# Optimization experiments

Measured on AMD Instinct MI355X. Metric: run time of the kernel, lower is better.

Reference implementation:

```python
import jax, jax.numpy as jnp
import numpy as np

IC, IND, MID, OC, OD, ITERS = 8, 16, 32, 8, 16, 3
B, H, W = 8, 64, 64


def squash(x, axis):
    sq = jnp.sum(x * x, axis=axis, keepdims=True)
    return sq / (0.5 + sq) * x / (jnp.sqrt(sq + 1e-6) + 1e-6)


def gconv(x, w, b, pad):
    # grouped conv over the IC capsule groups (equivalent to the per-capsule
    # Conv2d blocks applied to slices of the capsule axis)
    y = jax.lax.conv_general_dilated(
        x, w, (1, 1), pad,
        dimension_numbers=("NCHW", "OIHW", "NCHW"),
        feature_group_count=IC)
    return y + b[None, :, None, None]


def setup_inputs() -> dict:
    key = jax.random.key(0)
    ks = jax.random.split(key, 7)
    x = jax.random.normal(ks[0], (B, IC * IND, H, W), jnp.float32)
    w1 = jax.random.normal(ks[1], (IC * MID, IND, 1, 1), jnp.float32) * 0.1
    b1 = jax.random.normal(ks[2], (IC * MID,), jnp.float32) * 0.1
    w2 = jax.random.normal(ks[3], (IC * MID, MID, 3, 3), jnp.float32) * 0.05
    b2 = jax.random.normal(ks[4], (IC * MID,), jnp.float32) * 0.1
    w3 = jax.random.normal(ks[5], (IC * OC * OD, MID, 1, 1), jnp.float32) * 0.05
    b3 = jax.random.normal(ks[6], (IC * OC * OD,), jnp.float32) * 0.1
    attn_w = jnp.zeros((1, OC, 1, 1, 1), jnp.float32)  # torch init: zeros
    attn_b = jnp.ones((1, OC, 1, 1, 1), jnp.float32)   # torch init: ones
    return dict(x=x, w1=w1, b1=b1, w2=w2, b2=b2, w3=w3, b3=b3,
                attn_w=attn_w, attn_b=attn_b)


def reference(x, w1, b1, w2, b2, w3, b3, attn_w, attn_b):
    bsz = x.shape[0]
    h_, w_ = x.shape[-2], x.shape[-1]
    # per-capsule conv stack: ReLU -> 1x1 -> ReLU -> 3x3 -> ReLU -> 1x1
    h = jax.nn.relu(x)
    h = jax.nn.relu(gconv(h, w1, b1, "VALID"))
    h = jax.nn.relu(gconv(h, w2, b2, "SAME"))
    h = gconv(h, w3, b3, "VALID")                     # [B, IC*OC*OD, H, W]
    u_hat = h.reshape(bsz, IC, OC, OD, h_, w_)
    u_sq = squash(u_hat, axis=3)
    # dynamic routing
    b = jnp.zeros((bsz, IC, OC, h_, w_), u_hat.dtype)
    for _ in range(ITERS - 1):
        c = jax.nn.sigmoid(b)
        s = jnp.sum(u_sq * c[:, :, :, None], axis=1)   # [B, OC, OD, H, W]
        v = squash(s, axis=2)
        b = b + jnp.sum(u_sq * v[:, None], axis=3)     # [B, IC, OC, H, W]
    c = jax.nn.sigmoid(b)
    s = jnp.sum(u_hat * c[:, :, :, None], axis=1)      # [B, OC, OD, H, W]
    # SpatialCapsuleAttn
    mean_hw = jnp.mean(s, axis=(-2, -1), keepdims=True)        # adaptive avg pool(1)
    avg = jnp.sum(s * mean_hw, axis=2)                         # [B, OC, H, W]
    t = avg.reshape(bsz, OC, h_ * w_)
    m = jnp.mean(t, axis=-1, keepdims=True)
    sd = jnp.std(t, axis=-1, keepdims=True, ddof=1) + 1e-6     # torch std: unbiased
    t = (t - m) / sd
    t = t.reshape(bsz, OC, 1, h_, w_) * attn_w + attn_b
    s = s * jax.nn.sigmoid(t)
    out = s.reshape(bsz, OC * OD, h_, w_) + x
    return out
```

## Files before the change

### kernel.cpp

```cpp
#include <hip/hip_runtime.h>
#include <hip/hip_bf16.h>
#include <hip/hip_fp16.h>

#define HW 4096

typedef _Float16 f16x8 __attribute__((ext_vector_type(8)));
typedef float f32x4 __attribute__((ext_vector_type(4)));

#define FOR8(X) X(0) X(1) X(2) X(3) X(4) X(5) X(6) X(7)

static __device__ __forceinline__ __half2 u2h(unsigned int u) {
    union { unsigned int u; __half2 h; } c; c.u = u; return c.h;
}
static __device__ __forceinline__ unsigned int h2u(__half2 h) {
    union { unsigned int u; __half2 h; } c; c.h = h; return c.u;
}
static __device__ __forceinline__ f16x8 uint4_as_f16x8(uint4 v) {
    union { uint4 u; f16x8 f; } c; c.u = v; return c.f;
}

__global__ __launch_bounds__(256) void k0b_w3h(const float* __restrict__ w3, ushort* __restrict__ w3h) {
    int gi = blockIdx.x * 256 + threadIdx.x;
    if (gi >= 32768) return;
    int j = gi & 7;
    int l = (gi >> 3) & 63;
    int p = gi >> 9;
    int ic = p >> 3, oc = p & 7;
    int od = l & 15;
    int m  = ((l >> 4) << 3) + j;
    __half h = __float2half(w3[(size_t)((ic * 128 + oc * 16 + od) * 32 + m)]);
    w3h[gi] = __half_as_ushort(h);
}

__global__ __launch_bounds__(256) void k0c_w2f(const float* __restrict__ w2, ushort* __restrict__ w2f) {
    int gi = blockIdx.x * 256 + threadIdx.x;
    if (gi >= 73728) return;
    int j   = gi & 7;
    int l   = (gi >> 3) & 63;
    int h   = (gi >> 9) & 1;
    int tap = (gi >> 10) % 9;
    int g   = gi / 9216;
    int co = h * 16 + (l & 15);
    int ci = ((l >> 4) << 3) + j;
    float v = w2[(size_t)((g * 32 + co) * 32 + ci) * 9 + tap];
    w2f[gi] = __half_as_ushort(__float2half(v));
}

__global__ __launch_bounds__(256) void k1_conv1(const float* __restrict__ x, const float* __restrict__ w1,
                                                const float* __restrict__ b1, ushort* __restrict__ h1g) {
    int bi = blockIdx.x;
    int chunk = bi & 15;
    int g = (bi >> 4) & 7;
    int b = bi >> 7;
    int pos = chunk * 256 + threadIdx.x;

    const float* xb = x + (size_t)(b * 128 + g * 16) * HW + pos;
    float xv[16];
#pragma unroll
    for (int i = 0; i < 16; ++i) xv[i] = fmaxf(xb[i * HW], 0.f);

    const float* wg = w1 + g * 32 * 16;
    const float* bg = b1 + g * 32;
    ushort hv[32];
#pragma unroll
    for (int m = 0; m < 32; ++m) {
        float acc = bg[m];
#pragma unroll
        for (int i = 0; i < 16; ++i) acc = fmaf(xv[i], wg[m * 16 + i], acc);
        hv[m] = __half_as_ushort(__float2half(fmaxf(acc, 0.f)));
    }
    ushort* hb = h1g + ((size_t)(b * 8 + g) * HW + pos) * 32;
#pragma unroll
    for (int q = 0; q < 4; ++q) *(uint4*)&hb[q * 8] = *(uint4*)&hv[q * 8];
}

__global__ __launch_bounds__(256) void k2_conv2(const ushort* __restrict__ h1g, const ushort* __restrict__ w2f,
                                                const float* __restrict__ b2, ushort* __restrict__ h2g) {
    int bi = blockIdx.x;
    int pt = bi & 63;
    int g  = (bi >> 6) & 7;
    int b  = bi >> 9;
    int t  = threadIdx.x;
    int w  = t >> 6, l = t & 63;
    int pxbase = pt * 64 + w * 16;
    int kgrp = l >> 4;

    int y = pxbase >> 6;
    int x = (pxbase & 63) + (l & 15);

    const ushort* hbase = h1g + (size_t)(b * 8 + g) * HW * 32;
    f16x8 Bf[9];
#pragma unroll
    for (int dy = -1; dy <= 1; ++dy) {
        int yy = y + dy;
        int yyc = yy < 0 ? 0 : (yy > 63 ? 63 : yy);
        bool rv = (yy >= 0) && (yy < 64);
#pragma unroll
        for (int dx = -1; dx <= 1; ++dx) {
            int xx = x + dx;
            int xc = xx < 0 ? 0 : (xx > 63 ? 63 : xx);
            uint4 v = *(const uint4*)&hbase[((yyc << 6) + xc) * 32 + kgrp * 8];
            bool ok = rv && (xx >= 0) && (xx < 64);
            v.x = ok ? v.x : 0u; v.y = ok ? v.y : 0u;
            v.z = ok ? v.z : 0u; v.w = ok ? v.w : 0u;
            Bf[(dy + 1) * 3 + (dx + 1)] = uint4_as_f16x8(v);
        }
    }

    const ushort* wg = w2f + (size_t)g * 9216;
    f16x8 Af[9][2];
#pragma unroll
    for (int tap = 0; tap < 9; ++tap)
#pragma unroll
        for (int h = 0; h < 2; ++h)
            Af[tap][h] = *(const f16x8*)&wg[((tap * 2 + h) * 64 + l) * 8];

    f32x4 acc[2];
#pragma unroll
    for (int h = 0; h < 2; ++h) {
        float4 bias = *(const float4*)(b2 + g * 32 + h * 16 + kgrp * 4);
        acc[h][0] = bias.x; acc[h][1] = bias.y; acc[h][2] = bias.z; acc[h][3] = bias.w;
    }
#pragma unroll
    for (int tap = 0; tap < 9; ++tap) {
#pragma unroll
        for (int h = 0; h < 2; ++h)
            acc[h] = __builtin_amdgcn_mfma_f32_16x16x32_f16(Af[tap][h], Bf[tap], acc[h], 0, 0, 0);
    }

    int px = pxbase + (l & 15);
    ushort* ob = h2g + ((size_t)(b * 8 + g) * HW + px) * 32;
#pragma unroll
    for (int h = 0; h < 2; ++h) {
        __half2 lo = __floats2half2_rn(fmaxf(acc[h][0], 0.f), fmaxf(acc[h][1], 0.f));
        __half2 hi = __floats2half2_rn(fmaxf(acc[h][2], 0.f), fmaxf(acc[h][3], 0.f));
        uint2 wv; wv.x = h2u(lo); wv.y = h2u(hi);
        *(uint2*)&ob[h * 16 + kgrp * 4] = wv;
    }
}

__global__ __launch_bounds__(512) void k3f_route(const ushort* __restrict__ h2g, const ushort* __restrict__ w3h,
                                                 const float* __restrict__ b3, ushort* __restrict__ sOut,
                                                 float* __restrict__ part) {
    __shared__ ushort us[32 * 1024];
    __shared__ float wred[8][16][8];
    int bid = blockIdx.x;
    int b   = bid >> 7;
    int px0 = (bid & 127) << 5;
    int t   = threadIdx.x;
    int w   = t >> 6, l = t & 63;

    {
        int ic = w;
        int lrow = l & 15, lk = l >> 4;
        f16x8 bf0 = *(const f16x8*)&h2g[(((size_t)(b * 8 + ic)) * HW + px0 + lrow) * 32 + lk * 8];
        f16x8 bf1 = *(const f16x8*)&h2g[(((size_t)(b * 8 + ic)) * HW + px0 + 16 + lrow) * 32 + lk * 8];
        int s0sw = (lrow & 15) << 3;
#pragma unroll
        for (int oc = 0; oc < 8; ++oc) {
            f16x8 af = *(const f16x8*)&w3h[((ic * 8 + oc) * 64 + l) * 8];
            float4 bv = *(const float4*)(b3 + ic * 128 + oc * 16 + lk * 4);
            f32x4 c0; c0[0] = bv.x; c0[1] = bv.y; c0[2] = bv.z; c0[3] = bv.w;
            int ch = ic * 128 + oc * 16 + lk * 4;
            f32x4 d0 = __builtin_amdgcn_mfma_f32_16x16x32_f16(af, bf0, c0, 0, 0, 0);
            uint2 wv0;
            wv0.x = h2u(__floats2half2_rn(d0[0], d0[1]));
            wv0.y = h2u(__floats2half2_rn(d0[2], d0[3]));
            *(uint2*)&us[lrow * 1024 + (ch ^ s0sw)] = wv0;
            f32x4 d1 = __builtin_amdgcn_mfma_f32_16x16x32_f16(af, bf1, c0, 0, 0, 0);
            uint2 wv1;
            wv1.x = h2u(__floats2half2_rn(d1[0], d1[1]));
            wv1.y = h2u(__floats2half2_rn(d1[2], d1[3]));
            *(uint2*)&us[(16 + lrow) * 1024 + (ch ^ s0sw)] = wv1;
        }
    }
    __syncthreads();

    int px  = t >> 4;
    int oc  = (t >> 1) & 7;
    int odh = t & 1;
    int ssw = (px & 15) << 3;
    const ushort* ur = &us[px * 1024];
#define LDQ(i) uint4 q##i = *(const uint4*)&ur[((i) * 128 + oc * 16 + odh * 8) ^ ssw];
    FOR8(LDQ)
#undef LDQ
    __syncthreads();

#define UNP(i) float2 f0 = __half22float2(u2h(q##i.x)), f1 = __half22float2(u2h(q##i.y)), \
                      f2 = __half22float2(u2h(q##i.z)), f3 = __half22float2(u2h(q##i.w));

#define SC(i) float sc##i; { UNP(i) \
        float sp = f0.x*f0.x + f0.y*f0.y + f1.x*f1.x + f1.y*f1.y \
                 + f2.x*f2.x + f2.y*f2.y + f3.x*f3.x + f3.y*f3.y; \
        sp += __shfl_xor(sp, 1); \
        sc##i = sp / ((0.5f + sp) * (sqrtf(sp + 1e-6f) + 1e-6f)); }
    FOR8(SC)
#undef SC

#define BRI(i) float br##i = 0.f;
    FOR8(BRI)
#undef BRI

    float s0, s1, s2, s3, s4, s5, s6, s7;
#pragma unroll
    for (int it = 0; it < 2; ++it) {
#define CSC(i) float cs##i = sc##i / (1.f + __expf(-br##i));
        FOR8(CSC)
#undef CSC
        s0 = s1 = s2 = s3 = s4 = s5 = s6 = s7 = 0.f;
#define SVA(i) { UNP(i) \
        s0 = fmaf(f0.x, cs##i, s0); s1 = fmaf(f0.y, cs##i, s1); \
        s2 = fmaf(f1.x, cs##i, s2); s3 = fmaf(f1.y, cs##i, s3); \
        s4 = fmaf(f2.x, cs##i, s4); s5 = fmaf(f2.y, cs##i, s5); \
        s6 = fmaf(f3.x, cs##i, s6); s7 = fmaf(f3.y, cs##i, s7); }
        FOR8(SVA)
#undef SVA
        float sp = s0*s0 + s1*s1 + s2*s2 + s3*s3 + s4*s4 + s5*s5 + s6*s6 + s7*s7;
        sp += __shfl_xor(sp, 1);
        float f = sp / ((0.5f + sp) * (sqrtf(sp + 1e-6f) + 1e-6f));
#define DOTD(i) { UNP(i) \
        float dp = f0.x*s0 + f0.y*s1 + f1.x*s2 + f1.y*s3 + f2.x*s4 + f2.y*s5 + f3.x*s6 + f3.y*s7; \
        dp += __shfl_xor(dp, 1); \
        br##i = fmaf(sc##i * f, dp, br##i); }
        FOR8(DOTD)
#undef DOTD
    }

#define CF(i) float cf##i = 1.f / (1.f + __expf(-br##i));
    FOR8(CF)
#undef CF
    s0 = s1 = s2 = s3 = s4 = s5 = s6 = s7 = 0.f;
#define FS(i) { UNP(i) \
        s0 = fmaf(f0.x, cf##i, s0); s1 = fmaf(f0.y, cf##i, s1); \
        s2 = fmaf(f1.x, cf##i, s2); s3 = fmaf(f1.y, cf##i, s3); \
        s4 = fmaf(f2.x, cf##i, s4); s5 = fmaf(f2.y, cf##i, s5); \
        s6 = fmaf(f3.x, cf##i, s6); s7 = fmaf(f3.y, cf##i, s7); }
    FOR8(FS)
#undef FS
#undef UNP

    {
        uint4 pk;
        pk.x = h2u(__floats2half2_rn(s0, s1));
        pk.y = h2u(__floats2half2_rn(s2, s3));
        pk.z = h2u(__floats2half2_rn(s4, s5));
        pk.w = h2u(__floats2half2_rn(s6, s7));
        *(uint4*)&us[px * 1024 + ((oc * 16 + odh * 8) ^ ssw)] = pk;
    }

    {
        float p0 = s0, p1 = s1, p2 = s2, p3 = s3, p4 = s4, p5 = s5, p6 = s6, p7 = s7;
#pragma unroll
        for (int m = 16; m <= 32; m <<= 1) {
            p0 += __shfl_xor(p0, m); p1 += __shfl_xor(p1, m);
            p2 += __shfl_xor(p2, m); p3 += __shfl_xor(p3, m);
            p4 += __shfl_xor(p4, m); p5 += __shfl_xor(p5, m);
            p6 += __shfl_xor(p6, m); p7 += __shfl_xor(p7, m);
        }
        if ((l & 48) == 0) {
            float* wr = wred[w][oc * 2 + odh];
            wr[0] = p0; wr[1] = p1; wr[2] = p2; wr[3] = p3;
            wr[4] = p4; wr[5] = p5; wr[6] = p6; wr[7] = p7;
        }
    }
    __syncthreads();

    {
        int oc2 = w;
        int pxw = l >> 1, half = l & 1;
        int ch2 = (oc2 * 16 + half * 8) ^ ((pxw & 15) << 3);
        uint4 v = *(const uint4*)&us[pxw * 1024 + ch2];
        ushort* sb = sOut + ((size_t)(b * 8 + oc2) * 4096 + px0 + pxw) * 16 + half * 8;
        *(uint4*)sb = v;
    }
    if (t < 128) {
        int comb = t >> 3, j = t & 7;
        float a = 0.f;
#pragma unroll
        for (int ww = 0; ww < 8; ++ww) a += wred[ww][comb][j];
        int oc3 = comb >> 1, odh3 = comb & 1;
        part[((size_t)(b * 8 + oc3) * 128 + (bid & 127)) * 16 + odh3 * 8 + j] = a;
    }
}

__global__ __launch_bounds__(256) void k4_avg(const ushort* __restrict__ sIn, const float* __restrict__ part,
                                              float* __restrict__ avg, float* __restrict__ stats) {
    __shared__ float mh[16];
    int bi = blockIdx.x;
    int chunk = bi & 15;
    int bo = bi >> 4;
    int t = threadIdx.x;
    int pos = chunk * 256 + t;

    if (t < 16) {
        float a = 0.f;
        for (int c = 0; c < 128; ++c) a += part[(size_t)(bo * 128 + c) * 16 + t];
        mh[t] = a * (1.f / 4096.f);
    }
    __syncthreads();

    const ushort* sb = sIn + ((size_t)bo * 4096 + pos) * 16;
    uint4 qa = *(const uint4*)&sb[0];
    uint4 qb = *(const uint4*)&sb[8];
    float2 f0 = __half22float2(u2h(qa.x)), f1 = __half22float2(u2h(qa.y));
    float2 f2 = __half22float2(u2h(qa.z)), f3 = __half22float2(u2h(qa.w));
    float2 f4 = __half22float2(u2h(qb.x)), f5 = __half22float2(u2h(qb.y));
    float2 f6 = __half22float2(u2h(qb.z)), f7 = __half22float2(u2h(qb.w));
    float a = f0.x * mh[0] + f0.y * mh[1] + f1.x * mh[2] + f1.y * mh[3]
            + f2.x * mh[4] + f2.y * mh[5] + f3.x * mh[6] + f3.y * mh[7]
            + f4.x * mh[8] + f4.y * mh[9] + f5.x * mh[10] + f5.y * mh[11]
            + f6.x * mh[12] + f6.y * mh[13] + f7.x * mh[14] + f7.y * mh[15];
    avg[(size_t)bo * 4096 + pos] = a;

    float p1 = a, p2 = a * a;
#pragma unroll
    for (int m = 1; m < 64; m <<= 1) {
        p1 += __shfl_xor(p1, m);
        p2 += __shfl_xor(p2, m);
    }
    if ((t & 63) == 0) {
        atomicAdd(&stats[bo * 2],     p1);
        atomicAdd(&stats[bo * 2 + 1], p2);
    }
}

__global__ __launch_bounds__(256) void k5_out(const ushort* __restrict__ sIn, const float* __restrict__ x,
                                              const float* __restrict__ avg, const float* __restrict__ stats,
                                              const float* __restrict__ aw, const float* __restrict__ ab,
                                              float* __restrict__ out) {
    int bi = blockIdx.x;
    int chunk = bi & 15;
    int bo = bi >> 4;
    int oc = bo & 7;
    int pos = chunk * 256 + threadIdx.x;

    float sum = stats[bo * 2], sumsq = stats[bo * 2 + 1];
    float m   = sum * (1.f / 4096.f);
    float var = (sumsq - 4096.f * m * m) * (1.f / 4095.f);
    float sd  = sqrtf(fmaxf(var, 0.f)) + 1e-6f;

    float t   = (avg[(size_t)bo * 4096 + pos] - m) / sd * aw[oc] + ab[oc];
    float sig = 1.f / (1.f + __expf(-t));

    const ushort* sb = sIn + ((size_t)bo * 4096 + pos) * 16;
    uint4 qa = *(const uint4*)&sb[0];
    uint4 qb = *(const uint4*)&sb[8];
    float2 f0 = __half22float2(u2h(qa.x)), f1 = __half22float2(u2h(qa.y));
    float2 f2 = __half22float2(u2h(qa.z)), f3 = __half22float2(u2h(qa.w));
    float2 f4 = __half22float2(u2h(qb.x)), f5 = __half22float2(u2h(qb.y));
    float2 f6 = __half22float2(u2h(qb.z)), f7 = __half22float2(u2h(qb.w));
    float sv[16] = {f0.x, f0.y, f1.x, f1.y, f2.x, f2.y, f3.x, f3.y,
                    f4.x, f4.y, f5.x, f5.y, f6.x, f6.y, f7.x, f7.y};

    const float* xb = x + (size_t)bo * 16 * HW + pos;
    float* ob = out + (size_t)bo * 16 * HW + pos;
#pragma unroll
    for (int od = 0; od < 16; ++od) ob[od * HW] = fmaf(sv[od], sig, xb[od * HW]);
}

extern "C" void kernel_launch(void* const* d_in, const int* in_sizes, int n_in,
                              void* d_out, int out_size, void* d_ws, size_t ws_size,
                              hipStream_t stream) {
    const float* x  = (const float*)d_in[0];
    const float* w1 = (const float*)d_in[1];
    const float* b1 = (const float*)d_in[2];
    const float* w2 = (const float*)d_in[3];
    const float* b2 = (const float*)d_in[4];
    const float* w3 = (const float*)d_in[5];
    const float* b3 = (const float*)d_in[6];
    const float* aw = (const float*)d_in[7];
    const float* ab = (const float*)d_in[8];

    float* ws      = (float*)d_ws;
    ushort* h1g    = (ushort*)ws;
    ushort* h2g    = (ushort*)(ws + 4194304);
    ushort* sbuf   = (ushort*)(ws + 8388608);
    float* avg     = ws + 8388608 + 2097152;
    float* part    = avg + 262144;
    float* stats   = part + 131072;
    ushort* w3h    = (ushort*)(stats + 128);
    ushort* w2f    = w3h + 32768;

    hipMemsetAsync(stats, 0, 128 * sizeof(float), stream);
    k0b_w3h  <<<128, 256, 0, stream>>>(w3, w3h);
    k0c_w2f  <<<288, 256, 0, stream>>>(w2, w2f);
    k1_conv1 <<<1024, 256, 0, stream>>>(x, w1, b1, h1g);
    k2_conv2 <<<4096, 256, 0, stream>>>(h1g, w2f, b2, h2g);
    k3f_route<<<1024, 512, 0, stream>>>(h2g, w3h, b3, sbuf, part);
    k4_avg   <<<1024, 256, 0, stream>>>(sbuf, part, avg, stats);
    k5_out   <<<1024, 256, 0, stream>>>(sbuf, x, avg, stats, aw, ab, (float*)d_out);
}
```

Before: 104.5 us.

## Fuse 1x1 conv into 3x3 conv via shared-memory halo rows and merge prep kernels

The first 1x1 grouped conv is now computed inside the 3x3 conv kernel. Each block computes three halo rows of h1 (66 columns each) into shared memory and then reads its MFMA B-fragments from there. This removes the 16 MB fp16 h1 round trip through global memory and one launch, and the two weight-prep kernels are merged into one launch. In exchange each h1 row is recomputed about three times, only 198 of 256 threads do the 1x1 work, and a barrier now separates the two phases.

```diff
diff --git a/kernel.cpp b/kernel.cpp
--- a/kernel.cpp
+++ b/kernel.cpp
@@ -15,105 +15,94 @@
 static __device__ __forceinline__ unsigned int h2u(__half2 h) {
     union { unsigned int u; __half2 h; } c; c.h = h; return c.u;
 }
-static __device__ __forceinline__ f16x8 uint4_as_f16x8(uint4 v) {
-    union { uint4 u; f16x8 f; } c; c.u = v; return c.f;
-}
-
-__global__ __launch_bounds__(256) void k0b_w3h(const float* __restrict__ w3, ushort* __restrict__ w3h) {
-    int gi = blockIdx.x * 256 + threadIdx.x;
-    if (gi >= 32768) return;
-    int j = gi & 7;
-    int l = (gi >> 3) & 63;
-    int p = gi >> 9;
-    int ic = p >> 3, oc = p & 7;
-    int od = l & 15;
-    int m  = ((l >> 4) << 3) + j;
-    __half h = __float2half(w3[(size_t)((ic * 128 + oc * 16 + od) * 32 + m)]);
-    w3h[gi] = __half_as_ushort(h);
-}
-
-__global__ __launch_bounds__(256) void k0c_w2f(const float* __restrict__ w2, ushort* __restrict__ w2f) {
-    int gi = blockIdx.x * 256 + threadIdx.x;
-    if (gi >= 73728) return;
-    int j   = gi & 7;
-    int l   = (gi >> 3) & 63;
-    int h   = (gi >> 9) & 1;
-    int tap = (gi >> 10) % 9;
-    int g   = gi / 9216;
-    int co = h * 16 + (l & 15);
-    int ci = ((l >> 4) << 3) + j;
-    float v = w2[(size_t)((g * 32 + co) * 32 + ci) * 9 + tap];
-    w2f[gi] = __half_as_ushort(__float2half(v));
-}
-
-__global__ __launch_bounds__(256) void k1_conv1(const float* __restrict__ x, const float* __restrict__ w1,
-                                                const float* __restrict__ b1, ushort* __restrict__ h1g) {
+
+__global__ __launch_bounds__(256) void k0_prep(const float* __restrict__ w3, ushort* __restrict__ w3h,
+                                               const float* __restrict__ w2, ushort* __restrict__ w2f) {
+    int bid = blockIdx.x;
+    int t = threadIdx.x;
+    if (bid < 128) {
+        int gi = bid * 256 + t;
+        int j = gi & 7;
+        int l = (gi >> 3) & 63;
+        int p = gi >> 9;
+        int ic = p >> 3, oc = p & 7;
+        int od = l & 15;
+        int m  = ((l >> 4) << 3) + j;
+        w3h[gi] = __half_as_ushort(__float2half(w3[(size_t)((ic * 128 + oc * 16 + od) * 32 + m)]));
+    } else {
+        int gi = (bid - 128) * 256 + t;
+        if (gi >= 73728) return;
+        int j   = gi & 7;
+        int l   = (gi >> 3) & 63;
+        int h   = (gi >> 9) & 1;
+        int tap = (gi >> 10) % 9;
+        int g   = gi / 9216;
+        int co = h * 16 + (l & 15);
+        int ci = ((l >> 4) << 3) + j;
+        w2f[gi] = __half_as_ushort(__float2half(w2[(size_t)((g * 32 + co) * 32 + ci) * 9 + tap]));
+    }
+}
+
+__global__ __launch_bounds__(256) void k12_conv(const float* __restrict__ x, const float* __restrict__ w1,
+                                                const float* __restrict__ b1, const ushort* __restrict__ w2f,
+                                                const float* __restrict__ b2, ushort* __restrict__ h2g) {
+    __shared__ ushort h1s[3][66][40];
+
     int bi = blockIdx.x;
-    int chunk = bi & 15;
-    int g = (bi >> 4) & 7;
-    int b = bi >> 7;
-    int pos = chunk * 256 + threadIdx.x;
-
-    const float* xb = x + (size_t)(b * 128 + g * 16) * HW + pos;
-    float xv[16];
-#pragma unroll
-    for (int i = 0; i < 16; ++i) xv[i] = fmaxf(xb[i * HW], 0.f);
-
-    const float* wg = w1 + g * 32 * 16;
-    const float* bg = b1 + g * 32;
-    ushort hv[32];
-#pragma unroll
-    for (int m = 0; m < 32; ++m) {
-        float acc = bg[m];
-#pragma unroll
-        for (int i = 0; i < 16; ++i) acc = fmaf(xv[i], wg[m * 16 + i], acc);
-        hv[m] = __half_as_ushort(__float2half(fmaxf(acc, 0.f)));
-    }
-    ushort* hb = h1g + ((size_t)(b * 8 + g) * HW + pos) * 32;
-#pragma unroll
-    for (int q = 0; q < 4; ++q) *(uint4*)&hb[q * 8] = *(uint4*)&hv[q * 8];
-}
-
-__global__ __launch_bounds__(256) void k2_conv2(const ushort* __restrict__ h1g, const ushort* __restrict__ w2f,
-                                                const float* __restrict__ b2, ushort* __restrict__ h2g) {
-    int bi = blockIdx.x;
-    int pt = bi & 63;
+    int y  = bi & 63;
     int g  = (bi >> 6) & 7;
     int b  = bi >> 9;
     int t  = threadIdx.x;
+
+    if (t < 198) {
+        int r  = t / 66;
+        int xi = t - r * 66;
+        int yy = y + r - 1;
+        int xx = xi - 1;
+        bool valid = (yy >= 0) && (yy < 64) && (xx >= 0) && (xx < 64);
+        ushort hv[32];
+        if (valid) {
+            const float* xb = x + (size_t)(b * 128 + g * 16) * HW + yy * 64 + xx;
+            float xv[16];
+#pragma unroll
+            for (int i = 0; i < 16; ++i) xv[i] = fmaxf(xb[i * HW], 0.f);
+            const float* wg = w1 + g * 512;
+            const float* bg = b1 + g * 32;
+#pragma unroll
+            for (int m = 0; m < 32; ++m) {
+                float acc = bg[m];
+#pragma unroll
+                for (int i = 0; i < 16; ++i) acc = fmaf(xv[i], wg[m * 16 + i], acc);
+                hv[m] = __half_as_ushort(__float2half(fmaxf(acc, 0.f)));
+            }
+        } else {
+#pragma unroll
+            for (int m = 0; m < 32; ++m) hv[m] = 0;
+        }
+        ushort* dst = &h1s[r][xi][0];
+#pragma unroll
+        for (int q = 0; q < 4; ++q) *(uint4*)&dst[q * 8] = *(uint4*)&hv[q * 8];
+    }
+    __syncthreads();
+
     int w  = t >> 6, l = t & 63;
-    int pxbase = pt * 64 + w * 16;
-    int kgrp = l >> 4;
-
-    int y = pxbase >> 6;
-    int x = (pxbase & 63) + (l & 15);
-
-    const ushort* hbase = h1g + (size_t)(b * 8 + g) * HW * 32;
+    int lrow = l & 15, kgrp = l >> 4;
+    int xcol = w * 16 + lrow;
+
     f16x8 Bf[9];
 #pragma unroll
-    for (int dy = -1; dy <= 1; ++dy) {
-        int yy = y + dy;
-        int yyc = yy < 0 ? 0 : (yy > 63 ? 63 : yy);
-        bool rv = (yy >= 0) && (yy < 64);
-#pragma unroll
-        for (int dx = -1; dx <= 1; ++dx) {
-            int xx = x + dx;
-            int xc = xx < 0 ? 0 : (xx > 63 ? 63 : xx);
-            uint4 v = *(const uint4*)&hbase[((yyc << 6) + xc) * 32 + kgrp * 8];
-            bool ok = rv && (xx >= 0) && (xx < 64);
-            v.x = ok ? v.x : 0u; v.y = ok ? v.y : 0u;
-            v.z = ok ? v.z : 0u; v.w = ok ? v.w : 0u;
-            Bf[(dy + 1) * 3 + (dx + 1)] = uint4_as_f16x8(v);
-        }
-    }
-
-    const ushort* wg = w2f + (size_t)g * 9216;
+    for (int dy = 0; dy < 3; ++dy)
+#pragma unroll
+        for (int dx = 0; dx < 3; ++dx)
+            Bf[dy * 3 + dx] = *(const f16x8*)&h1s[dy][xcol + dx][kgrp * 8];
+
+    const ushort* wg2 = w2f + (size_t)g * 9216;
     f16x8 Af[9][2];
 #pragma unroll
     for (int tap = 0; tap < 9; ++tap)
 #pragma unroll
         for (int h = 0; h < 2; ++h)
-            Af[tap][h] = *(const f16x8*)&wg[((tap * 2 + h) * 64 + l) * 8];
+            Af[tap][h] = *(const f16x8*)&wg2[((tap * 2 + h) * 64 + l) * 8];
 
     f32x4 acc[2];
 #pragma unroll
@@ -128,7 +117,7 @@
             acc[h] = __builtin_amdgcn_mfma_f32_16x16x32_f16(Af[tap][h], Bf[tap], acc[h], 0, 0, 0);
     }
 
-    int px = pxbase + (l & 15);
+    int px = y * 64 + xcol;
     ushort* ob = h2g + ((size_t)(b * 8 + g) * HW + px) * 32;
 #pragma unroll
     for (int h = 0; h < 2; ++h) {
@@ -372,20 +361,17 @@
     const float* ab = (const float*)d_in[8];
 
     float* ws      = (float*)d_ws;
-    ushort* h1g    = (ushort*)ws;
-    ushort* h2g    = (ushort*)(ws + 4194304);
-    ushort* sbuf   = (ushort*)(ws + 8388608);
-    float* avg     = ws + 8388608 + 2097152;
+    ushort* h2g    = (ushort*)ws;
+    ushort* sbuf   = (ushort*)(ws + 4194304);
+    float* avg     = ws + 4194304 + 2097152;
     float* part    = avg + 262144;
     float* stats   = part + 131072;
     ushort* w3h    = (ushort*)(stats + 128);
     ushort* w2f    = w3h + 32768;
 
     hipMemsetAsync(stats, 0, 128 * sizeof(float), stream);
-    k0b_w3h  <<<128, 256, 0, stream>>>(w3, w3h);
-    k0c_w2f  <<<288, 256, 0, stream>>>(w2, w2f);
-    k1_conv1 <<<1024, 256, 0, stream>>>(x, w1, b1, h1g);
-    k2_conv2 <<<4096, 256, 0, stream>>>(h1g, w2f, b2, h2g);
+    k0_prep  <<<416, 256, 0, stream>>>(w3, w3h, w2, w2f);
+    k12_conv <<<4096, 256, 0, stream>>>(x, w1, b1, w2f, b2, h2g);
     k3f_route<<<1024, 512, 0, stream>>>(h2g, w3h, b3, sbuf, part);
     k4_avg   <<<1024, 256, 0, stream>>>(sbuf, part, avg, stats);
     k5_out   <<<1024, 256, 0, stream>>>(sbuf, x, avg, stats, aw, ab, (float*)d_out);
```

Measured after the change: 94.33 us. 9.7% less time.
